# Performance work log

Measured on AMD Instinct MI355X. Metric: run time of the kernel, lower is better.

## Reference

```python
import jax, jax.numpy as jnp
import numpy as np

# Standard SMPL kinematic tree (24 joints)
PARENTS = np.array([-1, 0, 0, 0, 1, 2, 3, 4, 5, 6, 7, 8, 9, 9, 9, 12, 13, 14, 16, 17, 18, 19, 20, 21], dtype=np.int32)
B, V, J, NB = 1024, 6890, 24, 10  # batch, vertices, joints, betas


def _rodrigues(r):
    """Axis-angle (..., 3) -> rotation matrices (..., 3, 3)."""
    theta = jnp.sqrt(jnp.sum(r * r, axis=-1, keepdims=True) + 1e-8)
    axis = r / theta
    c = jnp.cos(theta)[..., None]
    s = jnp.sin(theta)[..., None]
    x, y, z = axis[..., 0], axis[..., 1], axis[..., 2]
    zeros = jnp.zeros_like(x)
    K = jnp.stack([zeros, -z, y, z, zeros, -x, -y, x, zeros], axis=-1).reshape(r.shape[:-1] + (3, 3))
    outer = axis[..., :, None] * axis[..., None, :]
    eye = jnp.eye(3, dtype=r.dtype)
    return c * eye + (1.0 - c) * outer + s * K


def setup_inputs() -> dict:
    key = jax.random.key(0)
    ks = jax.random.split(key, 9)
    shape = jax.random.normal(ks[0], (B, NB), dtype=jnp.float32)
    body_pose = jax.random.normal(ks[1], (B, J - 1, 3), dtype=jnp.float32) * 0.2
    pelvis_rotation = jax.random.normal(ks[2], (B, 3), dtype=jnp.float32) * 0.2
    global_translation = jax.random.normal(ks[3], (B, 3), dtype=jnp.float32)
    v_template = jax.random.normal(ks[4], (V, 3), dtype=jnp.float32) * 0.3
    shapedirs = jax.random.normal(ks[5], (V, 3, NB), dtype=jnp.float32) * 0.01
    posedirs = jax.random.normal(ks[6], ((J - 1) * 9, V * 3), dtype=jnp.float32) * 0.01
    lbs_weights = jax.nn.softmax(jax.random.normal(ks[7], (V, J), dtype=jnp.float32) * 4.0, axis=-1)
    J_regressor = jax.nn.softmax(jax.random.normal(ks[8], (J, V), dtype=jnp.float32) * 4.0, axis=-1)
    parents = jnp.asarray(PARENTS)
    return {"shape": shape, "body_pose": body_pose, "pelvis_rotation": pelvis_rotation,
            "global_translation": global_translation, "v_template": v_template,
            "shapedirs": shapedirs, "posedirs": posedirs, "lbs_weights": lbs_weights,
            "J_regressor": J_regressor, "parents": parents}


def reference(shape, body_pose, pelvis_rotation, global_translation,
              v_template, shapedirs, posedirs, lbs_weights, J_regressor, parents):
    b = shape.shape[0]
    dtype = shape.dtype
    # --- shape blendshapes ---
    v_shaped = v_template + jnp.einsum('bl,vcl->bvc', shape, shapedirs)        # (B, V, 3)
    joints = jnp.einsum('jv,bvc->bjc', J_regressor, v_shaped)                  # (B, J, 3)
    # --- pose rotations + pose blendshapes ---
    full_pose = jnp.concatenate([pelvis_rotation[:, None, :], body_pose], axis=1)  # (B, J, 3)
    rot = _rodrigues(full_pose)                                                # (B, J, 3, 3)
    pose_feat = (rot[:, 1:] - jnp.eye(3, dtype=dtype)).reshape(b, (J - 1) * 9)
    v_posed = v_shaped + (pose_feat @ posedirs).reshape(b, -1, 3)              # (B, V, 3)
    # --- forward kinematics along tree ---
    rel_joints = joints.at[:, 1:].add(-joints[:, PARENTS[1:]])                 # (B, J, 3)
    T = jnp.concatenate([rot, rel_joints[..., None]], axis=-1)                 # (B, J, 3, 4)
    bottom = jnp.broadcast_to(jnp.asarray([0, 0, 0, 1], dtype=dtype), (b, J, 1, 4))
    T = jnp.concatenate([T, bottom], axis=-2)                                  # (B, J, 4, 4)
    chain = [T[:, 0]]
    for j in range(1, J):
        chain.append(chain[int(PARENTS[j])] @ T[:, j])
    A = jnp.stack(chain, axis=1)                                               # (B, J, 4, 4)
    # --- remove rest-pose joint locations ---
    t_corr = A[..., :3, 3] - jnp.einsum('bjxy,bjy->bjx', A[..., :3, :3], joints)
    A_rel = A.at[..., :3, 3].set(t_corr)
    # --- linear blend skinning ---
    Tv = jnp.einsum('vj,bjxy->bvxy', lbs_weights, A_rel)                       # (B, V, 4, 4)
    verts = jnp.einsum('bvxy,bvy->bvx', Tv[..., :3, :3], v_posed) + Tv[..., :3, 3]
    return verts + global_translation[:, None, :]                              # (B, V, 3)
```

## Files before the change

### kernel.cpp

```cpp
#include <hip/hip_runtime.h>
#include <stdint.h>

#define V_   6890
#define N3   20670
#define NPAD 20736
#define VPAD 7168
#define J_   24
#define NB_  10
#define KP   207
#define KE   224
#define LDP  201

typedef __attribute__((ext_vector_type(8))) short bf16x8;
typedef __attribute__((ext_vector_type(4))) float f32x4;

__device__ __forceinline__ float bf2f(ushort u) {
    union { uint32_t u; float f; } cv; cv.u = ((uint32_t)u) << 16; return cv.f;
}
__device__ __forceinline__ ushort f2bf(float f) {
    union { float f; uint32_t u; } cv; cv.f = f;
    uint32_t u = cv.u;
    u += 0x7FFFu + ((u >> 16) & 1u);
    return (ushort)(u >> 16);
}

__global__ __launch_bounds__(256) void k_pre(const float* __restrict__ jreg,
                                             const float* __restrict__ vt,
                                             const float* __restrict__ sd,
                                             const float* __restrict__ pd,
                                             const float* __restrict__ lw,
                                             float* __restrict__ jsp,
                                             ushort* __restrict__ bt,
                                             ushort* __restrict__ w_hi,
                                             ushort* __restrict__ w_lo) {
    int g = blockIdx.x;
    int t = threadIdx.x;
    if (g < 336) {
        int j = g % 24, c = g / 24;
        float acc[33];
#pragma unroll
        for (int i = 0; i < 33; i++) acc[i] = 0.f;
#pragma unroll
        for (int it = 0; it < 2; it++) {
            int v = c * 512 + it * 256 + t;
            if (v < V_) {
                float w = jreg[(size_t)j * V_ + v];
                acc[0] += w * vt[v * 3 + 0];
                acc[1] += w * vt[v * 3 + 1];
                acc[2] += w * vt[v * 3 + 2];
                const float* sdv = sd + (size_t)v * 30;
#pragma unroll
                for (int i = 0; i < 30; i++) acc[3 + i] += w * sdv[i];
            }
        }
        __shared__ float red[256][11];
#pragma unroll 1
        for (int ch = 0; ch < 3; ch++) {
#pragma unroll
            for (int i = 0; i < 11; i++) red[t][i] = acc[ch * 11 + i];
            __syncthreads();
            for (int s = 128; s > 0; s >>= 1) {
                if (t < s) {
#pragma unroll
                    for (int i = 0; i < 11; i++) red[t][i] += red[t + s][i];
                }
                __syncthreads();
            }
            if (t < 11) jsp[(size_t)(j * 14 + c) * 33 + ch * 11 + t] = red[0][t];
            __syncthreads();
        }
    } else if (g < 336 + 81 * 28) {
        int gg = g - 336;
        int nblk = gg % 81, kblk = gg / 81;
        int n  = nblk * 256 + t;
        int k0 = kblk * 8;
        bool valid = n < N3;
        union { ushort s[8]; uint4 v; } u;
#pragma unroll
        for (int i = 0; i < 8; i++) {
            int k = k0 + i;
            float x = 0.f;
            if (valid) {
                if (k < KP)              x = pd[(size_t)k * N3 + n];
                else if (k < KP + NB_)   x = sd[(size_t)n * NB_ + (k - KP)];
                else if (k == KP + NB_)  x = vt[n];
            }
            u.s[i] = f2bf(x);
        }
        *(uint4*)(bt + (size_t)n * KE + k0) = u.v;
    } else {
        int i = (g - 336 - 81 * 28) * 256 + t;
        int v = i >> 5, j = i & 31;
        float x = (j < 24 && v < V_) ? lw[(size_t)v * 24 + j] : 0.f;
        ushort hi = f2bf(x);
        w_hi[i] = hi;
        w_lo[i] = f2bf(x - bf2f(hi));
    }
}

__global__ __launch_bounds__(64) void k_pose(const float* __restrict__ shape,
                                             const float* __restrict__ body_pose,
                                             const float* __restrict__ pelvis,
                                             const float* __restrict__ jsp,
                                             ushort* __restrict__ pfext,
                                             ushort* __restrict__ aT_hi,
                                             ushort* __restrict__ aT_lo,
                                             int Breal) {
    int b = blockIdx.x;
    int t = threadIdx.x;
    if (b >= Breal) {
        uint32_t* pz = (uint32_t*)(pfext + (size_t)b * KE);
        for (int i = t; i < KE / 2; i += 64) pz[i] = 0;
        return;
    }
    __shared__ float js_s[792];
    __shared__ float Rs[24][9];
    __shared__ float Js[24][3];
    __shared__ float As[24][12];

    for (int idx = t; idx < 792; idx += 64) {
        int j = idx / 33, i = idx - j * 33;
        float s = 0.f;
#pragma unroll
        for (int c = 0; c < 14; c++) s += jsp[(size_t)(j * 14 + c) * 33 + i];
        js_s[idx] = s;
    }
    __syncthreads();

    if (t < 24) {
        float rx, ry, rz;
        if (t == 0) {
            rx = pelvis[b * 3 + 0]; ry = pelvis[b * 3 + 1]; rz = pelvis[b * 3 + 2];
        } else {
            const float* p = body_pose + ((size_t)b * 23 + (t - 1)) * 3;
            rx = p[0]; ry = p[1]; rz = p[2];
        }
        float th = sqrtf(rx * rx + ry * ry + rz * rz + 1e-8f);
        float inv = 1.f / th;
        float x = rx * inv, y = ry * inv, z = rz * inv;
        float c = cosf(th), s = sinf(th), omc = 1.f - c;
        float R[9];
        R[0] = c + omc * x * x;     R[1] = omc * x * y - s * z; R[2] = omc * x * z + s * y;
        R[3] = omc * y * x + s * z; R[4] = c + omc * y * y;     R[5] = omc * y * z - s * x;
        R[6] = omc * z * x - s * y; R[7] = omc * z * y + s * x; R[8] = c + omc * z * z;
#pragma unroll
        for (int e = 0; e < 9; e++) Rs[t][e] = R[e];

        const float* jsj = js_s + t * 33;
        float sh[10];
#pragma unroll
        for (int l = 0; l < 10; l++) sh[l] = shape[b * 10 + l];
#pragma unroll
        for (int c2 = 0; c2 < 3; c2++) {
            float a = jsj[c2];
#pragma unroll
            for (int l = 0; l < 10; l++) a += sh[l] * jsj[3 + c2 * 10 + l];
            Js[t][c2] = a;
        }
        ushort* pf = pfext + (size_t)b * KE;
        if (t >= 1) {
#pragma unroll
            for (int e = 0; e < 9; e++) {
                float v = R[e] - ((e == 0 || e == 4 || e == 8) ? 1.f : 0.f);
                pf[(t - 1) * 9 + e] = f2bf(v);
            }
        } else {
            for (int l = 0; l < 10; l++) pf[KP + l] = f2bf(sh[l]);
            pf[KP + NB_] = 0x3F80;
            for (int k = KP + NB_ + 1; k < KE; k++) pf[k] = 0;
        }
    }
    __syncthreads();

    if (t < 12) {
        int row = t >> 2, col = t & 3;
        As[0][t] = (col < 3) ? Rs[0][row * 3 + col] : Js[0][row];
    }
    __syncthreads();
    const int par[24] = {-1,0,0,0,1,2,3,4,5,6,7,8,9,9,9,12,13,14,16,17,18,19,20,21};
#pragma unroll 1
    for (int j = 1; j < 24; j++) {
        int p = par[j];
        float val = 0.f;
        if (t < 12) {
            int row = t >> 2, col = t & 3;
            if (col < 3) {
                val = As[p][row * 4 + 0] * Rs[j][0 * 3 + col]
                    + As[p][row * 4 + 1] * Rs[j][1 * 3 + col]
                    + As[p][row * 4 + 2] * Rs[j][2 * 3 + col];
            } else {
                float relx = Js[j][0] - Js[p][0];
                float rely = Js[j][1] - Js[p][1];
                float relz = Js[j][2] - Js[p][2];
                val = As[p][row * 4 + 0] * relx + As[p][row * 4 + 1] * rely
                    + As[p][row * 4 + 2] * relz + As[p][row * 4 + 3];
            }
        }
        __syncthreads();
        if (t < 12) As[j][t] = val;
        __syncthreads();
    }
    if (t < 24) {
        float tc[3];
#pragma unroll
        for (int row = 0; row < 3; row++) {
            float r0 = As[t][row * 4 + 0], r1 = As[t][row * 4 + 1], r2 = As[t][row * 4 + 2];
            tc[row] = As[t][row * 4 + 3] - (r0 * Js[t][0] + r1 * Js[t][1] + r2 * Js[t][2]);
        }
        As[t][3] = tc[0]; As[t][7] = tc[1]; As[t][11] = tc[2];
    }
    __syncthreads();
    ushort* dh = aT_hi + (size_t)b * 512;
    ushort* dl = aT_lo + (size_t)b * 512;
    for (int i = t; i < 512; i += 64) {
        int e = i >> 5, j = i & 31;
        float val = (e < 12 && j < 24) ? As[j][e] : 0.f;
        ushort hi = f2bf(val);
        dh[i] = hi;
        dl[i] = f2bf(val - bf2f(hi));
    }
}

__global__ __launch_bounds__(256) void k_fused(const ushort* __restrict__ bt,
                                               const ushort* __restrict__ pfext,
                                               const ushort* __restrict__ aT_hi,
                                               const ushort* __restrict__ aT_lo,
                                               const ushort* __restrict__ w_hi,
                                               const ushort* __restrict__ w_lo,
                                               const float* __restrict__ trans,
                                               float* __restrict__ vert,
                                               int Breal) {
    int lane = threadIdx.x & 63;
    int wv   = threadIdx.x >> 6;
    int quad = lane >> 4;
    int m    = lane & 15;
    int vtile = blockIdx.x;
    int nbase = vtile * 192;
    int bblk  = blockIdx.y * 64;
    int bbase = bblk + wv * 16;

    __shared__ float posed[64][LDP];

    f32x4 acc[3][4];
#pragma unroll
    for (int f = 0; f < 3; f++)
#pragma unroll
        for (int gq = 0; gq < 4; gq++) acc[f][gq] = (f32x4){0.f, 0.f, 0.f, 0.f};

    const ushort* ap = bt + (size_t)(nbase + wv * 48 + m) * KE + quad * 8;
    const ushort* bp = pfext + (size_t)(bblk + m) * KE + quad * 8;
#pragma unroll 2
    for (int ks = 0; ks < 7; ks++) {
        bf16x8 av[3], bv[4];
#pragma unroll
        for (int f = 0; f < 3; f++)
            av[f] = *(const bf16x8*)(ap + (size_t)(f * 16) * KE + ks * 32);
#pragma unroll
        for (int gq = 0; gq < 4; gq++)
            bv[gq] = *(const bf16x8*)(bp + (size_t)(gq * 16) * KE + ks * 32);
#pragma unroll
        for (int f = 0; f < 3; f++)
#pragma unroll
            for (int gq = 0; gq < 4; gq++)
                acc[f][gq] = __builtin_amdgcn_mfma_f32_16x16x32_bf16(av[f], bv[gq], acc[f][gq], 0, 0, 0);
    }
#pragma unroll
    for (int f = 0; f < 3; f++)
#pragma unroll
        for (int gq = 0; gq < 4; gq++) {
            float* dst = &posed[gq * 16 + m][wv * 48 + f * 16 + quad * 4];
            dst[0] = acc[f][gq][0]; dst[1] = acc[f][gq][1];
            dst[2] = acc[f][gq][2]; dst[3] = acc[f][gq][3];
        }
    __syncthreads();

    bf16x8 Wh[4], Wl[4];
#pragma unroll
    for (int i = 0; i < 4; i++) {
        size_t offw = (size_t)((vtile * 4 + i) * 16 + m) * 32 + quad * 8;
        Wh[i] = *(const bf16x8*)(w_hi + offw);
        Wl[i] = *(const bf16x8*)(w_lo + offw);
    }

#pragma unroll 1
    for (int bb = 0; bb < 16; bb++) {
        int b = bbase + bb;
        if (b >= Breal) break;
        size_t aoff = (size_t)b * 512 + m * 32 + quad * 8;
        bf16x8 Ah = *(const bf16x8*)(aT_hi + aoff);
        bf16x8 Al = *(const bf16x8*)(aT_lo + aoff);
        float tq = (quad < 3) ? trans[b * 3 + quad] : 0.f;
        const float* pr = &posed[wv * 16 + bb][0];
        float* vrow = vert + (size_t)b * N3;
#pragma unroll
        for (int i = 0; i < 4; i++) {
            int vloc = i * 16 + m;
            int v = vtile * 64 + vloc;
            float p0 = pr[vloc * 3 + 0];
            float p1 = pr[vloc * 3 + 1];
            float p2 = pr[vloc * 3 + 2];
            f32x4 a2 = (f32x4){0.f, 0.f, 0.f, 0.f};
            a2 = __builtin_amdgcn_mfma_f32_16x16x32_bf16(Ah, Wh[i], a2, 0, 0, 0);
            a2 = __builtin_amdgcn_mfma_f32_16x16x32_bf16(Al, Wh[i], a2, 0, 0, 0);
            a2 = __builtin_amdgcn_mfma_f32_16x16x32_bf16(Ah, Wl[i], a2, 0, 0, 0);
            float res = a2[0] * p0 + a2[1] * p1 + a2[2] * p2 + a2[3] + tq;
            if (quad < 3 && v < V_)
                vrow[3 * v + quad] = res;
        }
    }
}

extern "C" void kernel_launch(void* const* d_in, const int* in_sizes, int n_in,
                              void* d_out, int out_size, void* d_ws, size_t ws_size,
                              hipStream_t stream) {
    const float* shape = (const float*)d_in[0];
    const float* bpose = (const float*)d_in[1];
    const float* pelv  = (const float*)d_in[2];
    const float* trans = (const float*)d_in[3];
    const float* vt    = (const float*)d_in[4];
    const float* sd    = (const float*)d_in[5];
    const float* pd    = (const float*)d_in[6];
    const float* lw    = (const float*)d_in[7];
    const float* jr    = (const float*)d_in[8];
    float* out = (float*)d_out;

    int B    = in_sizes[0] / NB_;
    int Bpad = (B + 63) & ~63;

    char* ws = (char*)d_ws;
    size_t off = 0;
    auto alloc = [&](size_t bytes) { char* p = ws + off; off += (bytes + 255) & ~(size_t)255; return p; };
    float*  jsp   = (float*) alloc(24 * 14 * 33 * 4);
    ushort* pfext = (ushort*)alloc((size_t)Bpad * KE * 2);
    ushort* aT_hi = (ushort*)alloc((size_t)B * 512 * 2);
    ushort* aT_lo = (ushort*)alloc((size_t)B * 512 * 2);
    ushort* w_hi  = (ushort*)alloc((size_t)VPAD * 32 * 2);
    ushort* w_lo  = (ushort*)alloc((size_t)VPAD * 32 * 2);
    ushort* bt    = (ushort*)alloc((size_t)NPAD * KE * 2);

    k_pre<<<336 + 81 * 28 + VPAD * 32 / 256, 256, 0, stream>>>(jr, vt, sd, pd, lw,
                                                               jsp, bt, w_hi, w_lo);
    k_pose<<<Bpad, 64, 0, stream>>>(shape, bpose, pelv, jsp, pfext, aT_hi, aT_lo, B);
    k_fused<<<dim3(108, Bpad / 64), 256, 0, stream>>>(bt, pfext, aT_hi, aT_lo,
                                                      w_hi, w_lo, trans, out, B);
}
```

Measured before the change: 207.7 us.

## Transpose posedirs through LDS and remap fused grid for XCD locality

The bt conversion in the prep kernel now stages a 64-column by 224-row tile in shared memory. Reads are coalesced along n, and each thread then writes a 16-byte row chunk, where before each thread made strided 8-element gathers. The fused kernel changes to a 1D grid whose block index is remapped so that blocks landing on the same XCD share vertex tiles and batch blocks. This is meant to improve L2 reuse of bt and pfext. The remap only applies when there are 16 batch blocks; other sizes fall back to a plain mapping.

```diff
diff --git a/kernel.cpp b/kernel.cpp
--- a/kernel.cpp
+++ b/kernel.cpp
@@ -69,27 +69,32 @@
             if (t < 11) jsp[(size_t)(j * 14 + c) * 33 + ch * 11 + t] = red[0][t];
             __syncthreads();
         }
-    } else if (g < 336 + 81 * 28) {
-        int gg = g - 336;
-        int nblk = gg % 81, kblk = gg / 81;
-        int n  = nblk * 256 + t;
-        int k0 = kblk * 8;
-        bool valid = n < N3;
-        union { ushort s[8]; uint4 v; } u;
-#pragma unroll
-        for (int i = 0; i < 8; i++) {
-            int k = k0 + i;
+    } else if (g < 336 + 324) {
+        int nb = g - 336;
+        __shared__ ushort T[224][65];
+        for (int idx = t; idx < 64 * 224; idx += 256) {
+            int n0 = idx & 63;
+            int k  = idx >> 6;
+            int n  = nb * 64 + n0;
             float x = 0.f;
-            if (valid) {
+            if (n < N3) {
                 if (k < KP)              x = pd[(size_t)k * N3 + n];
                 else if (k < KP + NB_)   x = sd[(size_t)n * NB_ + (k - KP)];
                 else if (k == KP + NB_)  x = vt[n];
             }
-            u.s[i] = f2bf(x);
-        }
-        *(uint4*)(bt + (size_t)n * KE + k0) = u.v;
+            T[k][n0] = f2bf(x);
+        }
+        __syncthreads();
+        for (int c = t; c < 64 * 28; c += 256) {
+            int n0 = c / 28;
+            int k0 = (c - n0 * 28) * 8;
+            union { ushort s[8]; uint4 v; } u;
+#pragma unroll
+            for (int i = 0; i < 8; i++) u.s[i] = T[k0 + i][n0];
+            *(uint4*)(bt + (size_t)(nb * 64 + n0) * KE + k0) = u.v;
+        }
     } else {
-        int i = (g - 336 - 81 * 28) * 256 + t;
+        int i = (g - 336 - 324) * 256 + t;
         int v = i >> 5, j = i & 31;
         float x = (j < 24 && v < V_) ? lw[(size_t)v * 24 + j] : 0.f;
         ushort hi = f2bf(x);
@@ -229,14 +234,27 @@
                                                const ushort* __restrict__ w_lo,
                                                const float* __restrict__ trans,
                                                float* __restrict__ vert,
-                                               int Breal) {
+                                               int Breal, int NYB) {
     int lane = threadIdx.x & 63;
     int wv   = threadIdx.x >> 6;
     int quad = lane >> 4;
     int m    = lane & 15;
-    int vtile = blockIdx.x;
+
+    int bid = blockIdx.x;
+    int vtile, by;
+    if (NYB == 16) {
+        int xcd = bid & 7;
+        int r   = bid >> 3;
+        int rv  = r % 27;
+        vtile = (xcd & 3) * 27 + rv;
+        by    = (xcd >> 2) * 8 + r / 27;
+    } else {
+        vtile = bid % 108;
+        by    = bid / 108;
+    }
+
     int nbase = vtile * 192;
-    int bblk  = blockIdx.y * 64;
+    int bblk  = by * 64;
     int bbase = bblk + wv * 16;
 
     __shared__ float posed[64][LDP];
@@ -326,6 +344,7 @@
 
     int B    = in_sizes[0] / NB_;
     int Bpad = (B + 63) & ~63;
+    int NYB  = Bpad / 64;
 
     char* ws = (char*)d_ws;
     size_t off = 0;
@@ -338,9 +357,9 @@
     ushort* w_lo  = (ushort*)alloc((size_t)VPAD * 32 * 2);
     ushort* bt    = (ushort*)alloc((size_t)NPAD * KE * 2);
 
-    k_pre<<<336 + 81 * 28 + VPAD * 32 / 256, 256, 0, stream>>>(jr, vt, sd, pd, lw,
-                                                               jsp, bt, w_hi, w_lo);
+    k_pre<<<336 + 324 + VPAD * 32 / 256, 256, 0, stream>>>(jr, vt, sd, pd, lw,
+                                                           jsp, bt, w_hi, w_lo);
     k_pose<<<Bpad, 64, 0, stream>>>(shape, bpose, pelv, jsp, pfext, aT_hi, aT_lo, B);
-    k_fused<<<dim3(108, Bpad / 64), 256, 0, stream>>>(bt, pfext, aT_hi, aT_lo,
-                                                      w_hi, w_lo, trans, out, B);
-}
+    k_fused<<<dim3(108 * NYB), 256, 0, stream>>>(bt, pfext, aT_hi, aT_lo,
+                                                 w_hi, w_lo, trans, out, B, NYB);
+}
```

After: 211.6 us. No clear change (+1.9%).
